# Performance work log

Hardware: AMD Instinct MI355X
Metric: run time of the kernel (lower is better)

The kernel has to match this reference:

```python
import jax, jax.numpy as jnp
import numpy as np

I, H, B, T = 17, 128, 32768, 19

def setup_inputs() -> dict:
    key = jax.random.key(0)
    ks = jax.random.split(key, 7)
    s = 1.0 / np.sqrt(H)  # PyTorch LSTMCell/Linear init scale
    u = lambda k, shape: jax.random.uniform(k, shape, jnp.float32, -s, s)
    return {
        "x": jax.random.normal(ks[0], (B, T, I), jnp.float32),
        "W_ih": u(ks[1], (4 * H, I)),
        "W_hh": u(ks[2], (4 * H, H)),
        "b_ih": u(ks[3], (4 * H,)),
        "b_hh": u(ks[4], (4 * H,)),
        "W_out": u(ks[5], (I, H)),
        "b_out": u(ks[6], (I,)),
    }

def reference(x, W_ih, W_hh, b_ih, b_hh, W_out, b_out):
    B_, T_, _ = x.shape
    Hh = W_hh.shape[1]
    # Precompute input projections for all timesteps in one GEMM: [B,T,4H]
    x_proj = jnp.einsum('bti,gi->btg', x, W_ih) + b_ih + b_hh

    def step(carry, xp_t):
        h, c = carry
        gates = xp_t + h @ W_hh.T            # [B,4H]
        i_g, f_g, g_g, o_g = jnp.split(gates, 4, axis=-1)
        c = jax.nn.sigmoid(f_g) * c + jax.nn.sigmoid(i_g) * jnp.tanh(g_g)
        h = jax.nn.sigmoid(o_g) * jnp.tanh(c)
        y = h @ W_out.T + b_out              # [B,I]
        return (h, c), y

    h0 = jnp.zeros((B_, Hh), x.dtype)
    c0 = jnp.zeros((B_, Hh), x.dtype)
    _, ys = jax.lax.scan(step, (h0, c0), jnp.swapaxes(x_proj, 0, 1))  # ys: [T,B,I]
    return jnp.swapaxes(ys, 0, 1)  # [B,T,I]
```

## Files before the change

### kernel.cpp

```cpp
#include <hip/hip_runtime.h>

#define I_DIM 17
#define H_DIM 128
#define T_DIM 19
#define B_DIM 32768
#define M_ROWS 128
#define NTHR 512
#define GRID (B_DIM / M_ROWS)
#define XI 323
#define NF (M_ROWS * XI)
#define XSLOT 4352

#define GB0 0
#define GB1 16384
#define OFF_X 32768
#define OFF_WO 115456
#define LDS_TOT 123648

typedef __bf16 bf16x8 __attribute__((ext_vector_type(8)));
typedef float f32x4 __attribute__((ext_vector_type(4)));
typedef float f32x4u __attribute__((ext_vector_type(4), aligned(4)));
union FragU { bf16x8 v; unsigned short s[8]; uint4 u; };

#define K1 1.4426950408889634f
#define K2 2.8853900817779268f

__device__ __forceinline__ unsigned short f2bf(float f) {
    union { float f; unsigned u; } x; x.f = f;
    return (unsigned short)((x.u + 0x8000u) >> 16);
}

#define MFMA_Q(QT_, GB_, XB_, XK_, REC_) do {                                     \
    _Pragma("unroll") for (int g = 0; g < 4; ++g)                                 \
        acc[QT_][g] = bias[g];                                                    \
    FragU fx; fx.u = (uint4){0u, 0u, 0u, 0u};                                     \
    if (q < 2)                                                                    \
        fx.v = *(const bf16x8*)(smem + (XB_) + (QT_) * 512);                      \
    else if (q == 2)                                                              \
        fx.s[0] = *(const unsigned short*)(smem + (XK_) + (QT_) * 32);            \
    _Pragma("unroll") for (int g = 0; g < 4; ++g)                                 \
        acc[QT_][g] = __builtin_amdgcn_mfma_f32_16x16x32_bf16(wihr[g], fx.v, acc[QT_][g], 0, 0, 0); \
    if (REC_) {                                                                   \
        _Pragma("unroll") for (int kk = 0; kk < 4; ++kk) {                        \
            bf16x8 a = *(const bf16x8*)(smem + vkk[kk] + ((GB_) + (QT_) * 4096)); \
            _Pragma("unroll") for (int g = 0; g < 4; ++g)                         \
                acc[QT_][g] = __builtin_amdgcn_mfma_f32_16x16x32_bf16(whh[kk][g], a, acc[QT_][g], 0, 0, 0); \
        }                                                                         \
    }                                                                             \
} while (0)

#define ELEM_Q(QT_, GB_, CST_) do {                                               \
    unsigned long long hp = 0ull;                                                 \
    _Pragma("unroll") for (int r = 0; r < 4; ++r) {                               \
        float ui = __builtin_amdgcn_exp2f(acc[QT_][0][r]);                        \
        float uf = __builtin_amdgcn_exp2f(acc[QT_][1][r]);                        \
        float vg = __builtin_amdgcn_exp2f(acc[QT_][2][r]);                        \
        float uo = __builtin_amdgcn_exp2f(acc[QT_][3][r]);                        \
        float A_ = 1.f + ui, F_ = 1.f + uf, G_ = 1.f + vg;                        \
        float AG = A_ * G_;                                                       \
        int ci = (QT_) * 4 + r;                                                   \
        float c = (CST_[ci] * AG + (1.f - vg) * F_) * __builtin_amdgcn_rcpf(F_ * AG); \
        CST_[ci] = c;                                                             \
        float vc = __builtin_amdgcn_exp2f(-K2 * c);                               \
        float h = (1.f - vc) * __builtin_amdgcn_rcpf((1.f + uo) * (1.f + vc));    \
        union { float f; unsigned u; } hu; hu.f = h;                              \
        hp |= (unsigned long long)((hu.u + 0x8000u) >> 16) << (16 * r);           \
    }                                                                             \
    *(unsigned long long*)(smem + vwrT + ((GB_) + (QT_) * 4096)) = hp;            \
} while (0)

#define Y_T(GB_, YP_) do {                                                        \
    f32x4 ya = {0.f, 0.f, 0.f, 0.f};                                              \
    _Pragma("unroll") for (int kk = 0; kk < 4; ++kk) {                            \
        bf16x8 wa = *(const bf16x8*)(smem + vwo + kk * 1024);                     \
        bf16x8 hb = *(const bf16x8*)(smem + vkk[kk] + ((GB_) + 0) + yrt4);        \
        ya = __builtin_amdgcn_mfma_f32_16x16x32_bf16(wa, hb, ya, 0, 0, 0);        \
    }                                                                             \
    if (yct == 0) {                                                               \
        *(f32x4u*)(YP_) = ya + ybo;                                               \
    } else if (q == 0) {                                                          \
        (YP_)[0] = ya[0] + ybo[0];                                                \
    }                                                                             \
} while (0)

__global__ __launch_bounds__(NTHR)
__attribute__((amdgpu_waves_per_eu(2, 2)))
void flowlstm(
    const float* __restrict__ x, const float* __restrict__ W_ih,
    const float* __restrict__ W_hh, const float* __restrict__ b_ih,
    const float* __restrict__ b_hh, const float* __restrict__ W_out,
    const float* __restrict__ b_out, float* __restrict__ out)
{
    __shared__ __align__(16) unsigned char smem[LDS_TOT];
    const int tid = threadIdx.x;
    const int w = tid >> 6, lane = tid & 63, l15 = lane & 15, q = lane >> 4;
    const int cg = w;
    const int b0 = blockIdx.x * M_ROWS;

    {
        const float* xb = x + (size_t)b0 * XI;
        for (int j = 0; j < 81; ++j) {
            int f = tid + j * NTHR;
            if (f < NF) {
                float v = xb[f];
                unsigned uf_ = (unsigned)f;
                unsigned row = (uf_ * 51943u) >> 24;
                unsigned s = uf_ - row * 323u;
                unsigned t = (s * 61681u) >> 20;
                unsigned k = s - t * 17u;
                unsigned a;
                if (k == 16) a = OFF_X + t * XSLOT + 4096 + row * 2;
                else a = OFF_X + t * XSLOT + (row >> 4) * 512 + (k >> 3) * 256
                       + (row & 15) * 16 + (k & 7) * 2;
                *(unsigned short*)(smem + a) = f2bf(v);
            }
        }
    }
    {
        int ln = tid & 63, f = tid >> 6;
        int kk = f & 3, ct = f >> 2;
        int o = ct * 16 + (ln & 15);
        int kb = kk * 32 + (ln >> 4) * 8;
        FragU fu;
        #pragma unroll
        for (int e = 0; e < 8; ++e)
            fu.s[e] = (o < I_DIM) ? f2bf(W_out[o * H_DIM + kb + e]) : (unsigned short)0;
        *(uint4*)(smem + OFF_WO + f * 1024 + ln * 16) = fu.u;
    }
    float gsc[4] = { -K1, -K1, -K2, -K1 };

    bf16x8 whh[4][4];
    #pragma unroll
    for (int kk = 0; kk < 4; ++kk)
        #pragma unroll
        for (int g = 0; g < 4; ++g) {
            int n = g * H_DIM + cg * 16 + l15;
            const float* s = W_hh + n * H_DIM + kk * 32 + q * 8;
            FragU fu;
            #pragma unroll
            for (int e = 0; e < 8; ++e) fu.s[e] = f2bf(s[e] * gsc[g]);
            whh[kk][g] = fu.v;
        }
    bf16x8 wihr[4];
    #pragma unroll
    for (int g = 0; g < 4; ++g) {
        int n = g * H_DIM + cg * 16 + l15;
        FragU fu;
        #pragma unroll
        for (int e = 0; e < 8; ++e) {
            int k = q * 8 + e;
            fu.s[e] = (k < I_DIM) ? f2bf(W_ih[n * I_DIM + k] * gsc[g]) : (unsigned short)0;
        }
        wihr[g] = fu.v;
    }
    f32x4 bias[4];
    #pragma unroll
    for (int g = 0; g < 4; ++g)
        #pragma unroll
        for (int r = 0; r < 4; ++r) {
            int col = g * H_DIM + cg * 16 + 4 * q + r;
            bias[g][r] = (b_ih[col] + b_hh[col]) * gsc[g];
        }
    const unsigned xr7 = (unsigned)((l15 & 7) << 4);
    unsigned vkk[4];
    #pragma unroll
    for (int kk = 0; kk < 4; ++kk)
        vkk[kk] = (unsigned)(l15 * 256 + ((kk * 64 + q * 16) ^ xr7));
    const unsigned vwrT = (unsigned)(l15 * 256 + (((cg * 16 + 4 * q) * 2) ^ xr7));
    const int yct = w & 1;
    const unsigned yrt4 = (unsigned)((w >> 1) * 4096);
    const unsigned vwo = (unsigned)(OFF_WO + yct * 4096 + lane * 16);
    f32x4 ybo;
    #pragma unroll
    for (int r = 0; r < 4; ++r) {
        int col = yct * 16 + 4 * q + r;
        ybo[r] = b_out[col < I_DIM ? col : 16];
    }
    unsigned xyA  = (unsigned)(OFF_X + (q < 2 ? q * 256 : 0) + l15 * 16);
    unsigned xk16 = (unsigned)(OFF_X + 4096 + l15 * 2);
    float* ypG0 = out + (size_t)(b0 + (w >> 1) * 16 + l15) * XI + (yct ? 16 : 4 * q);
    float* ypG1 = ypG0 + (size_t)64 * XI;

    float cstA[16], cstB[16];
    #pragma unroll
    for (int i = 0; i < 16; ++i) { cstA[i] = 0.f; cstB[i] = 0.f; }

    f32x4 acc[4][4];

    __syncthreads();

    MFMA_Q(0, GB0, xyA, xk16, 0);
    MFMA_Q(1, GB0, xyA, xk16, 0);
    MFMA_Q(2, GB0, xyA, xk16, 0);
    MFMA_Q(3, GB0, xyA, xk16, 0);
    __syncthreads();
    ELEM_Q(0, GB0, cstA); MFMA_Q(0, GB1, xyA + 2048, xk16 + 128, 0);
    ELEM_Q(1, GB0, cstA); MFMA_Q(1, GB1, xyA + 2048, xk16 + 128, 0);
    ELEM_Q(2, GB0, cstA); MFMA_Q(2, GB1, xyA + 2048, xk16 + 128, 0);
    ELEM_Q(3, GB0, cstA); MFMA_Q(3, GB1, xyA + 2048, xk16 + 128, 0);
    __syncthreads();
    xyA += XSLOT; xk16 += XSLOT;

    #pragma unroll 1
    for (int k = 1; k < T_DIM; ++k) {
        ELEM_Q(0, GB1, cstB); MFMA_Q(0, GB0, xyA, xk16, 1);
        ELEM_Q(1, GB1, cstB); MFMA_Q(1, GB0, xyA, xk16, 1);
        Y_T(GB0, ypG0);
        ELEM_Q(2, GB1, cstB); MFMA_Q(2, GB0, xyA, xk16, 1);
        ELEM_Q(3, GB1, cstB); MFMA_Q(3, GB0, xyA, xk16, 1);
        __syncthreads();
        ELEM_Q(0, GB0, cstA); MFMA_Q(0, GB1, xyA + 2048, xk16 + 128, 1);
        ELEM_Q(1, GB0, cstA); MFMA_Q(1, GB1, xyA + 2048, xk16 + 128, 1);
        Y_T(GB1, ypG1);
        ELEM_Q(2, GB0, cstA); MFMA_Q(2, GB1, xyA + 2048, xk16 + 128, 1);
        ELEM_Q(3, GB0, cstA); MFMA_Q(3, GB1, xyA + 2048, xk16 + 128, 1);
        __syncthreads();
        xyA += XSLOT; xk16 += XSLOT;
        ypG0 += I_DIM; ypG1 += I_DIM;
    }

    ELEM_Q(0, GB1, cstB);
    ELEM_Q(1, GB1, cstB);
    Y_T(GB0, ypG0);
    ELEM_Q(2, GB1, cstB);
    ELEM_Q(3, GB1, cstB);
    __syncthreads();
    Y_T(GB1, ypG1);
}

extern "C" void kernel_launch(void* const* d_in, const int* in_sizes, int n_in,
                              void* d_out, int out_size, void* d_ws, size_t ws_size,
                              hipStream_t stream) {
    const float* x     = (const float*)d_in[0];
    const float* W_ih  = (const float*)d_in[1];
    const float* W_hh  = (const float*)d_in[2];
    const float* b_ih  = (const float*)d_in[3];
    const float* b_hh  = (const float*)d_in[4];
    const float* W_out = (const float*)d_in[5];
    const float* b_out = (const float*)d_in[6];
    float* out = (float*)d_out;

    dim3 grid(GRID), block(NTHR);
    flowlstm<<<grid, block, 0, stream>>>(x, W_ih, W_hh, b_ih, b_hh, W_out, b_out, out);
}
```

Measured before the change: 151.1 us.

## Halve rows per block, move W_hh into LDS, stream x per timestep

Each block now handles 64 batch rows with 1024 threads instead of 128 rows with 512 threads. W_hh moves from per-wave registers into LDS and is re-read each step. The bias is folded into the W_ih MFMA through a constant-one input column. x is no longer bulk-staged up front; each step prefetches the next timestep into a double-buffered LDS slot. The two interleaved half-batches in flight are replaced by a single step sequence with two barriers per step, aiming for more waves per SIMD and less register pressure, at the cost of extra LDS traffic and more synchronisation.

```diff
diff --git a/kernel.cpp b/kernel.cpp
--- a/kernel.cpp
+++ b/kernel.cpp
@@ -4,18 +4,17 @@
 #define H_DIM 128
 #define T_DIM 19
 #define B_DIM 32768
-#define M_ROWS 128
-#define NTHR 512
+#define M_ROWS 64
+#define NTHR 1024
 #define GRID (B_DIM / M_ROWS)
 #define XI 323
-#define NF (M_ROWS * XI)
-#define XSLOT 4352
-
-#define GB0 0
-#define GB1 16384
-#define OFF_X 32768
-#define OFF_WO 115456
-#define LDS_TOT 123648
+#define XSLOT 2176
+
+#define OFF_WHH 0
+#define OFF_H   131072
+#define OFF_X   147456
+#define OFF_WO  151808
+#define LDS_TOT 160000
 
 typedef __bf16 bf16x8 __attribute__((ext_vector_type(8)));
 typedef float f32x4 __attribute__((ext_vector_type(4)));
@@ -30,61 +29,88 @@
     return (unsigned short)((x.u + 0x8000u) >> 16);
 }
 
-#define MFMA_Q(QT_, GB_, XB_, XK_, REC_) do {                                     \
-    _Pragma("unroll") for (int g = 0; g < 4; ++g)                                 \
-        acc[QT_][g] = bias[g];                                                    \
-    FragU fx; fx.u = (uint4){0u, 0u, 0u, 0u};                                     \
-    if (q < 2)                                                                    \
-        fx.v = *(const bf16x8*)(smem + (XB_) + (QT_) * 512);                      \
-    else if (q == 2)                                                              \
-        fx.s[0] = *(const unsigned short*)(smem + (XK_) + (QT_) * 32);            \
-    _Pragma("unroll") for (int g = 0; g < 4; ++g)                                 \
-        acc[QT_][g] = __builtin_amdgcn_mfma_f32_16x16x32_bf16(wihr[g], fx.v, acc[QT_][g], 0, 0, 0); \
+#define STEP_READ(P_, REC_) do {                                                  \
+    _Pragma("unroll") for (int tile = 0; tile < 2; ++tile) {                      \
+        FragU fx; fx.u = (uint4){0u, 0u, 0u, 0u};                                 \
+        if (q < 2)                                                                \
+            fx.v = *(const bf16x8*)(smem + xyA + ((P_) * XSLOT + tile * 512));    \
+        else if (q == 2) {                                                        \
+            fx.s[0] = *(const unsigned short*)(smem + xk16 + ((P_) * XSLOT + tile * 32)); \
+            fx.s[1] = (unsigned short)0x3F80;                \
+        }                                                                         \
+        _Pragma("unroll") for (int g = 0; g < 4; ++g) {                           \
+            f32x4 z = {0.f, 0.f, 0.f, 0.f};                                       \
+            acc[tile][g] = __builtin_amdgcn_mfma_f32_16x16x32_bf16(wihr[g], fx.v, z, 0, 0, 0); \
+        }                                                                         \
+    }                                                                             \
     if (REC_) {                                                                   \
         _Pragma("unroll") for (int kk = 0; kk < 4; ++kk) {                        \
-            bf16x8 a = *(const bf16x8*)(smem + vkk[kk] + ((GB_) + (QT_) * 4096)); \
+            bf16x8 aw[4];                                                         \
             _Pragma("unroll") for (int g = 0; g < 4; ++g)                         \
-                acc[QT_][g] = __builtin_amdgcn_mfma_f32_16x16x32_bf16(whh[kk][g], a, acc[QT_][g], 0, 0, 0); \
-        }                                                                         \
-    }                                                                             \
-} while (0)
-
-#define ELEM_Q(QT_, GB_, CST_) do {                                               \
+                aw[g] = *(const bf16x8*)(smem + vwhh + (kk * 4096 + g * 1024));   \
+            _Pragma("unroll") for (int tile = 0; tile < 2; ++tile) {              \
+                bf16x8 hb = *(const bf16x8*)(smem + vkk[kk] + tile * 4096);       \
+                _Pragma("unroll") for (int g = 0; g < 4; ++g)                     \
+                    acc[tile][g] = __builtin_amdgcn_mfma_f32_16x16x32_bf16(aw[g], hb, acc[tile][g], 0, 0, 0); \
+            }                                                                     \
+        }                                                                         \
+    }                                                                             \
+} while (0)
+
+#define ELEM_T(TILE_) do {                                                        \
     unsigned long long hp = 0ull;                                                 \
     _Pragma("unroll") for (int r = 0; r < 4; ++r) {                               \
-        float ui = __builtin_amdgcn_exp2f(acc[QT_][0][r]);                        \
-        float uf = __builtin_amdgcn_exp2f(acc[QT_][1][r]);                        \
-        float vg = __builtin_amdgcn_exp2f(acc[QT_][2][r]);                        \
-        float uo = __builtin_amdgcn_exp2f(acc[QT_][3][r]);                        \
+        float ui = __builtin_amdgcn_exp2f(acc[TILE_][0][r]);                      \
+        float uf = __builtin_amdgcn_exp2f(acc[TILE_][1][r]);                      \
+        float vg = __builtin_amdgcn_exp2f(acc[TILE_][2][r]);                      \
+        float uo = __builtin_amdgcn_exp2f(acc[TILE_][3][r]);                      \
         float A_ = 1.f + ui, F_ = 1.f + uf, G_ = 1.f + vg;                        \
         float AG = A_ * G_;                                                       \
-        int ci = (QT_) * 4 + r;                                                   \
-        float c = (CST_[ci] * AG + (1.f - vg) * F_) * __builtin_amdgcn_rcpf(F_ * AG); \
-        CST_[ci] = c;                                                             \
+        int ci = (TILE_) * 4 + r;                                                 \
+        float c = (cst[ci] * AG + (1.f - vg) * F_) * __builtin_amdgcn_rcpf(F_ * AG); \
+        cst[ci] = c;                                                              \
         float vc = __builtin_amdgcn_exp2f(-K2 * c);                               \
         float h = (1.f - vc) * __builtin_amdgcn_rcpf((1.f + uo) * (1.f + vc));    \
         union { float f; unsigned u; } hu; hu.f = h;                              \
         hp |= (unsigned long long)((hu.u + 0x8000u) >> 16) << (16 * r);           \
     }                                                                             \
-    *(unsigned long long*)(smem + vwrT + ((GB_) + (QT_) * 4096)) = hp;            \
-} while (0)
-
-#define Y_T(GB_, YP_) do {                                                        \
-    f32x4 ya = {0.f, 0.f, 0.f, 0.f};                                              \
-    _Pragma("unroll") for (int kk = 0; kk < 4; ++kk) {                            \
-        bf16x8 wa = *(const bf16x8*)(smem + vwo + kk * 1024);                     \
-        bf16x8 hb = *(const bf16x8*)(smem + vkk[kk] + ((GB_) + 0) + yrt4);        \
-        ya = __builtin_amdgcn_mfma_f32_16x16x32_bf16(wa, hb, ya, 0, 0, 0);        \
-    }                                                                             \
-    if (yct == 0) {                                                               \
-        *(f32x4u*)(YP_) = ya + ybo;                                               \
-    } else if (q == 0) {                                                          \
-        (YP_)[0] = ya[0] + ybo[0];                                                \
-    }                                                                             \
+    *(unsigned long long*)(smem + vwrT + (TILE_) * 4096) = hp;                    \
+} while (0)
+
+#define Y_BURST() do {                                                            \
+    if (w < 8) {                                                                  \
+        f32x4 ya = {0.f, 0.f, 0.f, 0.f};                                          \
+        _Pragma("unroll") for (int kk = 0; kk < 4; ++kk) {                        \
+            bf16x8 wa = *(const bf16x8*)(smem + vwo + kk * 1024);                 \
+            bf16x8 hb = *(const bf16x8*)(smem + yv[kk]);                          \
+            ya = __builtin_amdgcn_mfma_f32_16x16x32_bf16(wa, hb, ya, 0, 0, 0);    \
+        }                                                                         \
+        if (yct == 0) {                                                           \
+            *(f32x4u*)ypt = ya + ybo;                                             \
+        } else if (q == 0) {                                                      \
+            ypt[0] = ya[0] + ybo[0];                                              \
+        }                                                                         \
+        ypt += I_DIM;                                                             \
+    }                                                                             \
+} while (0)
+
+#define STEP(T_, P_, REC_) do {                                                   \
+    float xr1 = 0.f, xr2 = 0.f;                                                   \
+    const bool pf = (T_) + 1 < T_DIM;                                             \
+    if (pf) { xr1 = xp1[17]; if (xv2) xr2 = xp2[17]; }                            \
+    xp1 += 17; xp2 += 17;                                                         \
+    STEP_READ(P_, REC_);                                                          \
+    if (REC_) { Y_BURST(); __syncthreads(); }                \
+    ELEM_T(0); ELEM_T(1);                                                         \
+    if (pf) {                                                                     \
+        *(unsigned short*)(smem + xd1 + (1 - (P_)) * XSLOT) = f2bf(xr1);          \
+        if (xv2) *(unsigned short*)(smem + xd2 + (1 - (P_)) * XSLOT) = f2bf(xr2); \
+    }                                                                             \
+    __syncthreads();                                \
 } while (0)
 
 __global__ __launch_bounds__(NTHR)
-__attribute__((amdgpu_waves_per_eu(2, 2)))
+__attribute__((amdgpu_waves_per_eu(4, 4)))
 void flowlstm(
     const float* __restrict__ x, const float* __restrict__ W_ih,
     const float* __restrict__ W_hh, const float* __restrict__ b_ih,
@@ -94,29 +120,23 @@
     __shared__ __align__(16) unsigned char smem[LDS_TOT];
     const int tid = threadIdx.x;
     const int w = tid >> 6, lane = tid & 63, l15 = lane & 15, q = lane >> 4;
-    const int cg = w;
+    const int mh = w >> 3, cg = w & 7;
     const int b0 = blockIdx.x * M_ROWS;
 
-    {
-        const float* xb = x + (size_t)b0 * XI;
-        for (int j = 0; j < 81; ++j) {
-            int f = tid + j * NTHR;
-            if (f < NF) {
-                float v = xb[f];
-                unsigned uf_ = (unsigned)f;
-                unsigned row = (uf_ * 51943u) >> 24;
-                unsigned s = uf_ - row * 323u;
-                unsigned t = (s * 61681u) >> 20;
-                unsigned k = s - t * 17u;
-                unsigned a;
-                if (k == 16) a = OFF_X + t * XSLOT + 4096 + row * 2;
-                else a = OFF_X + t * XSLOT + (row >> 4) * 512 + (k >> 3) * 256
-                       + (row & 15) * 16 + (k & 7) * 2;
-                *(unsigned short*)(smem + a) = f2bf(v);
-            }
-        }
-    }
-    {
+    #pragma unroll
+    for (int i = 0; i < 8; ++i) {
+        int s = tid + i * NTHR;
+        int ln = s & 63, f = s >> 6;
+        int g = f & 3, kk = (f >> 2) & 3, cgs = f >> 4;
+        float sc = (g == 2) ? -K2 : -K1;
+        int n = g * H_DIM + cgs * 16 + (ln & 15);
+        const float* sp = W_hh + n * H_DIM + kk * 32 + (ln >> 4) * 8;
+        FragU fu;
+        #pragma unroll
+        for (int e = 0; e < 8; ++e) fu.s[e] = f2bf(sp[e] * sc);
+        *(uint4*)(smem + OFF_WHH + f * 1024 + ln * 16) = fu.u;
+    }
+    if (tid < 512) {
         int ln = tid & 63, f = tid >> 6;
         int kk = f & 3, ct = f >> 2;
         int o = ct * 16 + (ln & 15);
@@ -127,48 +147,34 @@
             fu.s[e] = (o < I_DIM) ? f2bf(W_out[o * H_DIM + kb + e]) : (unsigned short)0;
         *(uint4*)(smem + OFF_WO + f * 1024 + ln * 16) = fu.u;
     }
-    float gsc[4] = { -K1, -K1, -K2, -K1 };
-
-    bf16x8 whh[4][4];
-    #pragma unroll
-    for (int kk = 0; kk < 4; ++kk)
-        #pragma unroll
-        for (int g = 0; g < 4; ++g) {
-            int n = g * H_DIM + cg * 16 + l15;
-            const float* s = W_hh + n * H_DIM + kk * 32 + q * 8;
-            FragU fu;
-            #pragma unroll
-            for (int e = 0; e < 8; ++e) fu.s[e] = f2bf(s[e] * gsc[g]);
-            whh[kk][g] = fu.v;
-        }
     bf16x8 wihr[4];
     #pragma unroll
     for (int g = 0; g < 4; ++g) {
+        float sc = (g == 2) ? -K2 : -K1;
         int n = g * H_DIM + cg * 16 + l15;
         FragU fu;
         #pragma unroll
         for (int e = 0; e < 8; ++e) {
             int k = q * 8 + e;
-            fu.s[e] = (k < I_DIM) ? f2bf(W_ih[n * I_DIM + k] * gsc[g]) : (unsigned short)0;
+            float v = 0.f;
+            if (k < I_DIM)       v = W_ih[n * I_DIM + k] * sc;
+            else if (k == I_DIM) v = (b_ih[n] + b_hh[n]) * sc;
+            fu.s[e] = f2bf(v);
         }
         wihr[g] = fu.v;
     }
-    f32x4 bias[4];
-    #pragma unroll
-    for (int g = 0; g < 4; ++g)
-        #pragma unroll
-        for (int r = 0; r < 4; ++r) {
-            int col = g * H_DIM + cg * 16 + 4 * q + r;
-            bias[g][r] = (b_ih[col] + b_hh[col]) * gsc[g];
-        }
     const unsigned xr7 = (unsigned)((l15 & 7) << 4);
-    unsigned vkk[4];
+    unsigned vkk[4], yv[4];
     #pragma unroll
     for (int kk = 0; kk < 4; ++kk)
-        vkk[kk] = (unsigned)(l15 * 256 + ((kk * 64 + q * 16) ^ xr7));
-    const unsigned vwrT = (unsigned)(l15 * 256 + (((cg * 16 + 4 * q) * 2) ^ xr7));
+        vkk[kk] = (unsigned)(OFF_H + mh * 8192 + l15 * 256 + ((kk * 64 + q * 16) ^ xr7));
+    const unsigned vwrT = (unsigned)(OFF_H + mh * 8192 + l15 * 256 + (((cg * 16 + 4 * q) * 2) ^ xr7));
+    const unsigned vwhh = (unsigned)(OFF_WHH + cg * 16384 + lane * 16);
     const int yct = w & 1;
-    const unsigned yrt4 = (unsigned)((w >> 1) * 4096);
+    const unsigned ytile = (unsigned)((w >> 1) * 4096);
+    #pragma unroll
+    for (int kk = 0; kk < 4; ++kk)
+        yv[kk] = (unsigned)(OFF_H + ytile + l15 * 256 + ((kk * 64 + q * 16) ^ xr7));
     const unsigned vwo = (unsigned)(OFF_WO + yct * 4096 + lane * 16);
     f32x4 ybo;
     #pragma unroll
@@ -176,56 +182,56 @@
         int col = yct * 16 + 4 * q + r;
         ybo[r] = b_out[col < I_DIM ? col : 16];
     }
-    unsigned xyA  = (unsigned)(OFF_X + (q < 2 ? q * 256 : 0) + l15 * 16);
-    unsigned xk16 = (unsigned)(OFF_X + 4096 + l15 * 2);
-    float* ypG0 = out + (size_t)(b0 + (w >> 1) * 16 + l15) * XI + (yct ? 16 : 4 * q);
-    float* ypG1 = ypG0 + (size_t)64 * XI;
-
-    float cstA[16], cstB[16];
-    #pragma unroll
-    for (int i = 0; i < 16; ++i) { cstA[i] = 0.f; cstB[i] = 0.f; }
-
-    f32x4 acc[4][4];
+    const unsigned xyA  = (unsigned)(OFF_X + mh * 1024 + (q < 2 ? q * 256 : 0) + l15 * 16);
+    const unsigned xk16 = (unsigned)(OFF_X + 2048 + mh * 64 + l15 * 2);
+    float* ypt = out + (size_t)(b0 + (w >> 1) * 16 + l15) * XI + (yct ? 16 : 4 * q);
+
+    const unsigned row1 = ((unsigned)tid * 61681u) >> 20;
+    const unsigned k1 = (unsigned)tid - row1 * 17u;
+    const bool xv2 = tid < (M_ROWS * I_DIM - NTHR);
+    const unsigned f2v = (unsigned)(tid + NTHR);
+    const unsigned row2 = xv2 ? ((f2v * 61681u) >> 20) : 0u;
+    const unsigned k2 = xv2 ? (f2v - row2 * 17u) : 0u;
+    const unsigned xd1 = (k1 == 16) ? (unsigned)(OFF_X + 2048 + row1 * 2)
+        : (unsigned)(OFF_X + (row1 >> 4) * 512 + (k1 >> 3) * 256 + (row1 & 15) * 16 + (k1 & 7) * 2);
+    const unsigned xd2 = (k2 == 16) ? (unsigned)(OFF_X + 2048 + row2 * 2)
+        : (unsigned)(OFF_X + (row2 >> 4) * 512 + (k2 >> 3) * 256 + (row2 & 15) * 16 + (k2 & 7) * 2);
+    const float* xp1 = x + (size_t)(b0 + row1) * XI + k1;
+    const float* xp2 = x + (size_t)(b0 + row2) * XI + k2;
+
+    *(unsigned short*)(smem + xd1) = f2bf(xp1[0]);
+    if (xv2) *(unsigned short*)(smem + xd2) = f2bf(xp2[0]);
+
+    float cst[8];
+    #pragma unroll
+    for (int i = 0; i < 8; ++i) cst[i] = 0.f;
+
+    f32x4 acc[2][4];
 
     __syncthreads();
 
-    MFMA_Q(0, GB0, xyA, xk16, 0);
-    MFMA_Q(1, GB0, xyA, xk16, 0);
-    MFMA_Q(2, GB0, xyA, xk16, 0);
-    MFMA_Q(3, GB0, xyA, xk16, 0);
-    __syncthreads();
-    ELEM_Q(0, GB0, cstA); MFMA_Q(0, GB1, xyA + 2048, xk16 + 128, 0);
-    ELEM_Q(1, GB0, cstA); MFMA_Q(1, GB1, xyA + 2048, xk16 + 128, 0);
-    ELEM_Q(2, GB0, cstA); MFMA_Q(2, GB1, xyA + 2048, xk16 + 128, 0);
-    ELEM_Q(3, GB0, cstA); MFMA_Q(3, GB1, xyA + 2048, xk16 + 128, 0);
-    __syncthreads();
-    xyA += XSLOT; xk16 += XSLOT;
+    STEP(0, 0, 0);
 
     #pragma unroll 1
-    for (int k = 1; k < T_DIM; ++k) {
-        ELEM_Q(0, GB1, cstB); MFMA_Q(0, GB0, xyA, xk16, 1);
-        ELEM_Q(1, GB1, cstB); MFMA_Q(1, GB0, xyA, xk16, 1);
-        Y_T(GB0, ypG0);
-        ELEM_Q(2, GB1, cstB); MFMA_Q(2, GB0, xyA, xk16, 1);
-        ELEM_Q(3, GB1, cstB); MFMA_Q(3, GB0, xyA, xk16, 1);
-        __syncthreads();
-        ELEM_Q(0, GB0, cstA); MFMA_Q(0, GB1, xyA + 2048, xk16 + 128, 1);
-        ELEM_Q(1, GB0, cstA); MFMA_Q(1, GB1, xyA + 2048, xk16 + 128, 1);
-        Y_T(GB1, ypG1);
-        ELEM_Q(2, GB0, cstA); MFMA_Q(2, GB1, xyA + 2048, xk16 + 128, 1);
-        ELEM_Q(3, GB0, cstA); MFMA_Q(3, GB1, xyA + 2048, xk16 + 128, 1);
-        __syncthreads();
-        xyA += XSLOT; xk16 += XSLOT;
-        ypG0 += I_DIM; ypG1 += I_DIM;
-    }
-
-    ELEM_Q(0, GB1, cstB);
-    ELEM_Q(1, GB1, cstB);
-    Y_T(GB0, ypG0);
-    ELEM_Q(2, GB1, cstB);
-    ELEM_Q(3, GB1, cstB);
-    __syncthreads();
-    Y_T(GB1, ypG1);
+    for (int t = 1; t < T_DIM; t += 2) {
+        STEP(t, 1, 1);
+        STEP(t + 1, 0, 1);
+    }
+
+    if (w < 8) {
+        f32x4 ya = {0.f, 0.f, 0.f, 0.f};
+        #pragma unroll
+        for (int kk = 0; kk < 4; ++kk) {
+            bf16x8 wa = *(const bf16x8*)(smem + vwo + kk * 1024);
+            bf16x8 hb = *(const bf16x8*)(smem + yv[kk]);
+            ya = __builtin_amdgcn_mfma_f32_16x16x32_bf16(wa, hb, ya, 0, 0, 0);
+        }
+        if (yct == 0) {
+            *(f32x4u*)ypt = ya + ybo;
+        } else if (q == 0) {
+            ypt[0] = ya[0] + ybo[0];
+        }
+    }
 }
 
 extern "C" void kernel_launch(void* const* d_in, const int* in_sizes, int n_in,
```

Result: slower. 160.5 us (+6.3%).

## Switch LSTM recurrence to 32x32x16 MFMA tiles with single-step h ping-pong

Applied to the files above, without the earlier changes.

Rebuilds the recurrent GEMM around 32x32x16 bf16 MFMA. Each wave owns two 8-column gate slices across all four gates, giving 32-row gate tiles. The bias is folded into the input-projection MFMA through a constant-one K lane. The two interleaved half-batch pipelines are replaced by one full-batch step per barrier, with an h ping-pong buffer. W_out moves from LDS into registers, and the output projection is done once per step over both half-batches. The aim is higher MFMA efficiency and fewer LDS reads and barriers, at the cost of more registers, a larger LDS footprint, and less ILP between the elementwise and MFMA phases.

```diff
diff --git a/kernel.cpp b/kernel.cpp
--- a/kernel.cpp
+++ b/kernel.cpp
@@ -11,14 +11,13 @@
 #define NF (M_ROWS * XI)
 #define XSLOT 4352
 
-#define GB0 0
-#define GB1 16384
-#define OFF_X 32768
-#define OFF_WO 115456
-#define LDS_TOT 123648
+#define OFF_H 0
+#define OFF_X 65536
+#define LDS_TOT 148224
 
 typedef __bf16 bf16x8 __attribute__((ext_vector_type(8)));
 typedef float f32x4 __attribute__((ext_vector_type(4)));
+typedef float f32x16 __attribute__((ext_vector_type(16)));
 typedef float f32x4u __attribute__((ext_vector_type(4), aligned(4)));
 union FragU { bf16x8 v; unsigned short s[8]; uint4 u; };
 
@@ -30,57 +29,94 @@
     return (unsigned short)((x.u + 0x8000u) >> 16);
 }
 
-#define MFMA_Q(QT_, GB_, XB_, XK_, REC_) do {                                     \
-    _Pragma("unroll") for (int g = 0; g < 4; ++g)                                 \
-        acc[QT_][g] = bias[g];                                                    \
-    FragU fx; fx.u = (uint4){0u, 0u, 0u, 0u};                                     \
-    if (q < 2)                                                                    \
-        fx.v = *(const bf16x8*)(smem + (XB_) + (QT_) * 512);                      \
-    else if (q == 2)                                                              \
-        fx.s[0] = *(const unsigned short*)(smem + (XK_) + (QT_) * 32);            \
-    _Pragma("unroll") for (int g = 0; g < 4; ++g)                                 \
-        acc[QT_][g] = __builtin_amdgcn_mfma_f32_16x16x32_bf16(wihr[g], fx.v, acc[QT_][g], 0, 0, 0); \
+#define RB(BT_, P_) do {                                                          \
+    _Pragma("unroll") for (int kk = 0; kk < 8; ++kk)                              \
+        hb[kk] = *(const bf16x8*)(smem + OFF_H + (1 - (P_)) * 32768               \
+                 + ((BT_) * 32 + l31) * 256 + ((kk * 32 + hi * 16) ^ sw15));      \
+} while (0)
+
+#define MQ(BT_, CTI_, ACC_, REC_) do {                                            \
+    FragU f1; f1.v = *(const bf16x8*)(smem + xt + (BT_) * 1024 + lane * 16);      \
+    FragU f2; f2.u = (uint4){0u, 0u, 0u, 0u};                                     \
+    if (hi == 0) {                                                                \
+        f2.s[0] = *(const unsigned short*)(smem + xt + 4096 + ((BT_) * 32 + l31) * 2); \
+        f2.s[1] = (unsigned short)0x3F80;                                         \
+    }                                                                             \
+    f32x16 z = {0.f,0.f,0.f,0.f,0.f,0.f,0.f,0.f,0.f,0.f,0.f,0.f,0.f,0.f,0.f,0.f};\
+    ACC_ = __builtin_amdgcn_mfma_f32_32x32x16_bf16(wihr[CTI_][0], f1.v, z, 0, 0, 0); \
+    ACC_ = __builtin_amdgcn_mfma_f32_32x32x16_bf16(wihr[CTI_][1], f2.v, ACC_, 0, 0, 0); \
     if (REC_) {                                                                   \
-        _Pragma("unroll") for (int kk = 0; kk < 4; ++kk) {                        \
-            bf16x8 a = *(const bf16x8*)(smem + vkk[kk] + ((GB_) + (QT_) * 4096)); \
-            _Pragma("unroll") for (int g = 0; g < 4; ++g)                         \
-                acc[QT_][g] = __builtin_amdgcn_mfma_f32_16x16x32_bf16(whh[kk][g], a, acc[QT_][g], 0, 0, 0); \
-        }                                                                         \
-    }                                                                             \
-} while (0)
-
-#define ELEM_Q(QT_, GB_, CST_) do {                                               \
+        _Pragma("unroll") for (int kk = 0; kk < 8; ++kk)                          \
+            ACC_ = __builtin_amdgcn_mfma_f32_32x32x16_bf16(whh[CTI_][kk], hb[kk], ACC_, 0, 0, 0); \
+    }                                                                             \
+} while (0)
+
+#define EQ(ACC_, TI_, CTI_, BT_, P_) do {                                         \
     unsigned long long hp = 0ull;                                                 \
-    _Pragma("unroll") for (int r = 0; r < 4; ++r) {                               \
-        float ui = __builtin_amdgcn_exp2f(acc[QT_][0][r]);                        \
-        float uf = __builtin_amdgcn_exp2f(acc[QT_][1][r]);                        \
-        float vg = __builtin_amdgcn_exp2f(acc[QT_][2][r]);                        \
-        float uo = __builtin_amdgcn_exp2f(acc[QT_][3][r]);                        \
+    _Pragma("unroll") for (int jj = 0; jj < 4; ++jj) {                            \
+        float ui = __builtin_amdgcn_exp2f(ACC_[jj]);                              \
+        float uf = __builtin_amdgcn_exp2f(ACC_[4 + jj]);                          \
+        float vg = __builtin_amdgcn_exp2f(ACC_[8 + jj]);                          \
+        float uo = __builtin_amdgcn_exp2f(ACC_[12 + jj]);                         \
         float A_ = 1.f + ui, F_ = 1.f + uf, G_ = 1.f + vg;                        \
         float AG = A_ * G_;                                                       \
-        int ci = (QT_) * 4 + r;                                                   \
-        float c = (CST_[ci] * AG + (1.f - vg) * F_) * __builtin_amdgcn_rcpf(F_ * AG); \
-        CST_[ci] = c;                                                             \
+        int ci = (TI_) * 4 + jj;                                                  \
+        float c = (cst[ci] * AG + (1.f - vg) * F_) * __builtin_amdgcn_rcpf(F_ * AG); \
+        cst[ci] = c;                                                              \
         float vc = __builtin_amdgcn_exp2f(-K2 * c);                               \
         float h = (1.f - vc) * __builtin_amdgcn_rcpf((1.f + uo) * (1.f + vc));    \
         union { float f; unsigned u; } hu; hu.f = h;                              \
-        hp |= (unsigned long long)((hu.u + 0x8000u) >> 16) << (16 * r);           \
-    }                                                                             \
-    *(unsigned long long*)(smem + vwrT + ((GB_) + (QT_) * 4096)) = hp;            \
-} while (0)
-
-#define Y_T(GB_, YP_) do {                                                        \
-    f32x4 ya = {0.f, 0.f, 0.f, 0.f};                                              \
+        hp |= (unsigned long long)((hu.u + 0x8000u) >> 16) << (16 * jj);          \
+    }                                                                             \
+    *(unsigned long long*)(smem + OFF_H + (P_) * 32768 + ((BT_) * 32 + l31) * 256 \
+        + (((2 * w + (CTI_)) * 16 + hi * 8) ^ sw15)) = hp;                        \
+} while (0)
+
+#define YB(P_) do {                                                               \
+    f32x4 ya0 = {0.f,0.f,0.f,0.f}, ya1 = {0.f,0.f,0.f,0.f};                       \
     _Pragma("unroll") for (int kk = 0; kk < 4; ++kk) {                            \
-        bf16x8 wa = *(const bf16x8*)(smem + vwo + kk * 1024);                     \
-        bf16x8 hb = *(const bf16x8*)(smem + vkk[kk] + ((GB_) + 0) + yrt4);        \
-        ya = __builtin_amdgcn_mfma_f32_16x16x32_bf16(wa, hb, ya, 0, 0, 0);        \
+        bf16x8 h0 = *(const bf16x8*)(smem + OFF_H + (1 - (P_)) * 32768            \
+                   + (ybt * 16 + l15) * 256 + ((kk * 64 + q * 16) ^ (l15 << 4))); \
+        bf16x8 h1 = *(const bf16x8*)(smem + OFF_H + (1 - (P_)) * 32768            \
+                   + ((ybt + 4) * 16 + l15) * 256 + ((kk * 64 + q * 16) ^ (l15 << 4))); \
+        ya0 = __builtin_amdgcn_mfma_f32_16x16x32_bf16(wor[kk], h0, ya0, 0, 0, 0); \
+        ya1 = __builtin_amdgcn_mfma_f32_16x16x32_bf16(wor[kk], h1, ya1, 0, 0, 0); \
     }                                                                             \
     if (yct == 0) {                                                               \
-        *(f32x4u*)(YP_) = ya + ybo;                                               \
+        *(f32x4u*)ypt0 = ya0 + ybo;                                               \
+        *(f32x4u*)ypt1 = ya1 + ybo;                                               \
     } else if (q == 0) {                                                          \
-        (YP_)[0] = ya[0] + ybo[0];                                                \
-    }                                                                             \
+        ypt0[0] = ya0[0] + ybo[0];                                                \
+        ypt1[0] = ya1[0] + ybo[0];                                                \
+    }                                                                             \
+    ypt0 += I_DIM; ypt1 += I_DIM;                                                 \
+} while (0)
+
+#define STEP(P_, REC_) do {                                                       \
+    bf16x8 hb[8];                                                                 \
+    if (REC_) RB(0, P_);                                                          \
+    MQ(0, 0, accA, REC_);                                                         \
+    MQ(0, 1, accB, REC_);                                                         \
+    if (REC_) RB(1, P_);                                                          \
+    EQ(accA, 0, 0, 0, P_);                                                        \
+    MQ(1, 0, accA, REC_);                                                         \
+    EQ(accB, 1, 1, 0, P_);                                                        \
+    MQ(1, 1, accB, REC_);                                                         \
+    if (REC_) RB(2, P_);                                                          \
+    EQ(accA, 2, 0, 1, P_);                                                        \
+    MQ(2, 0, accA, REC_);                                                         \
+    EQ(accB, 3, 1, 1, P_);                                                        \
+    MQ(2, 1, accB, REC_);                                                         \
+    if (REC_) YB(P_);                                                             \
+    if (REC_) RB(3, P_);                                                          \
+    EQ(accA, 4, 0, 2, P_);                                                        \
+    MQ(3, 0, accA, REC_);                                                         \
+    EQ(accB, 5, 1, 2, P_);                                                        \
+    MQ(3, 1, accB, REC_);                                                         \
+    EQ(accA, 6, 0, 3, P_);                                                        \
+    EQ(accB, 7, 1, 3, P_);                                                        \
+    xt += XSLOT;                                                                  \
+    __syncthreads();                                                              \
 } while (0)
 
 __global__ __launch_bounds__(NTHR)
@@ -93,8 +129,9 @@
 {
     __shared__ __align__(16) unsigned char smem[LDS_TOT];
     const int tid = threadIdx.x;
-    const int w = tid >> 6, lane = tid & 63, l15 = lane & 15, q = lane >> 4;
-    const int cg = w;
+    const int w = tid >> 6, lane = tid & 63;
+    const int l31 = lane & 31, hi = lane >> 5, l15 = lane & 15, q = lane >> 4;
+    const unsigned sw15 = (unsigned)((l31 & 15) << 4);
     const int b0 = blockIdx.x * M_ROWS;
 
     {
@@ -109,123 +146,84 @@
                 unsigned t = (s * 61681u) >> 20;
                 unsigned k = s - t * 17u;
                 unsigned a;
-                if (k == 16) a = OFF_X + t * XSLOT + 4096 + row * 2;
-                else a = OFF_X + t * XSLOT + (row >> 4) * 512 + (k >> 3) * 256
-                       + (row & 15) * 16 + (k & 7) * 2;
+                if (k == 16u)
+                    a = OFF_X + t * XSLOT + 4096 + row * 2;
+                else
+                    a = OFF_X + t * XSLOT + (row >> 5) * 1024
+                      + (((k >> 3) * 32 + (row & 31)) * 16) + (k & 7) * 2;
                 *(unsigned short*)(smem + a) = f2bf(v);
             }
         }
     }
-    {
-        int ln = tid & 63, f = tid >> 6;
-        int kk = f & 3, ct = f >> 2;
-        int o = ct * 16 + (ln & 15);
-        int kb = kk * 32 + (ln >> 4) * 8;
+    bf16x8 whh[2][8];
+    const int jrow = l31 & 7, grow = l31 >> 3;
+    const float scl = (grow == 2) ? -K2 : -K1;
+    #pragma unroll
+    for (int cti = 0; cti < 2; ++cti) {
+        int n = grow * H_DIM + (2 * w + cti) * 8 + jrow;
+        #pragma unroll
+        for (int kk = 0; kk < 8; ++kk) {
+            const float* sp = W_hh + n * H_DIM + kk * 16 + hi * 8;
+            FragU fu;
+            #pragma unroll
+            for (int e = 0; e < 8; ++e) fu.s[e] = f2bf(sp[e] * scl);
+            whh[cti][kk] = fu.v;
+        }
+    }
+    bf16x8 wihr[2][2];
+    #pragma unroll
+    for (int cti = 0; cti < 2; ++cti) {
+        int n = grow * H_DIM + (2 * w + cti) * 8 + jrow;
+        FragU fa, fb;
+        #pragma unroll
+        for (int e = 0; e < 8; ++e) {
+            int k0 = hi * 8 + e;
+            fa.s[e] = f2bf(W_ih[n * I_DIM + k0] * scl);
+            int k1 = 16 + hi * 8 + e;
+            float v = 0.f;
+            if (k1 == 16)      v = W_ih[n * I_DIM + 16] * scl;
+            else if (k1 == 17) v = (b_ih[n] + b_hh[n]) * scl;
+            fb.s[e] = f2bf(v);
+        }
+        wihr[cti][0] = fa.v;
+        wihr[cti][1] = fb.v;
+    }
+    const int ybt = w >> 1, yct = w & 1;
+    const int ycol = yct * 16 + l15;
+    bf16x8 wor[4];
+    #pragma unroll
+    for (int kk = 0; kk < 4; ++kk) {
         FragU fu;
         #pragma unroll
         for (int e = 0; e < 8; ++e)
-            fu.s[e] = (o < I_DIM) ? f2bf(W_out[o * H_DIM + kb + e]) : (unsigned short)0;
-        *(uint4*)(smem + OFF_WO + f * 1024 + ln * 16) = fu.u;
-    }
-    float gsc[4] = { -K1, -K1, -K2, -K1 };
-
-    bf16x8 whh[4][4];
-    #pragma unroll
-    for (int kk = 0; kk < 4; ++kk)
-        #pragma unroll
-        for (int g = 0; g < 4; ++g) {
-            int n = g * H_DIM + cg * 16 + l15;
-            const float* s = W_hh + n * H_DIM + kk * 32 + q * 8;
-            FragU fu;
-            #pragma unroll
-            for (int e = 0; e < 8; ++e) fu.s[e] = f2bf(s[e] * gsc[g]);
-            whh[kk][g] = fu.v;
-        }
-    bf16x8 wihr[4];
-    #pragma unroll
-    for (int g = 0; g < 4; ++g) {
-        int n = g * H_DIM + cg * 16 + l15;
-        FragU fu;
-        #pragma unroll
-        for (int e = 0; e < 8; ++e) {
-            int k = q * 8 + e;
-            fu.s[e] = (k < I_DIM) ? f2bf(W_ih[n * I_DIM + k] * gsc[g]) : (unsigned short)0;
-        }
-        wihr[g] = fu.v;
-    }
-    f32x4 bias[4];
-    #pragma unroll
-    for (int g = 0; g < 4; ++g)
-        #pragma unroll
-        for (int r = 0; r < 4; ++r) {
-            int col = g * H_DIM + cg * 16 + 4 * q + r;
-            bias[g][r] = (b_ih[col] + b_hh[col]) * gsc[g];
-        }
-    const unsigned xr7 = (unsigned)((l15 & 7) << 4);
-    unsigned vkk[4];
-    #pragma unroll
-    for (int kk = 0; kk < 4; ++kk)
-        vkk[kk] = (unsigned)(l15 * 256 + ((kk * 64 + q * 16) ^ xr7));
-    const unsigned vwrT = (unsigned)(l15 * 256 + (((cg * 16 + 4 * q) * 2) ^ xr7));
-    const int yct = w & 1;
-    const unsigned yrt4 = (unsigned)((w >> 1) * 4096);
-    const unsigned vwo = (unsigned)(OFF_WO + yct * 4096 + lane * 16);
+            fu.s[e] = (ycol < I_DIM) ? f2bf(W_out[ycol * H_DIM + kk * 32 + q * 8 + e])
+                                     : (unsigned short)0;
+        wor[kk] = fu.v;
+    }
     f32x4 ybo;
     #pragma unroll
     for (int r = 0; r < 4; ++r) {
         int col = yct * 16 + 4 * q + r;
         ybo[r] = b_out[col < I_DIM ? col : 16];
     }
-    unsigned xyA  = (unsigned)(OFF_X + (q < 2 ? q * 256 : 0) + l15 * 16);
-    unsigned xk16 = (unsigned)(OFF_X + 4096 + l15 * 2);
-    float* ypG0 = out + (size_t)(b0 + (w >> 1) * 16 + l15) * XI + (yct ? 16 : 4 * q);
-    float* ypG1 = ypG0 + (size_t)64 * XI;
-
-    float cstA[16], cstB[16];
-    #pragma unroll
-    for (int i = 0; i < 16; ++i) { cstA[i] = 0.f; cstB[i] = 0.f; }
-
-    f32x4 acc[4][4];
+    float* ypt0 = out + (size_t)(b0 + ybt * 16 + l15) * XI + (yct ? 16 : 4 * q);
+    float* ypt1 = ypt0 + (size_t)64 * XI;
+
+    float cst[32];
+    #pragma unroll
+    for (int i = 0; i < 32; ++i) cst[i] = 0.f;
+    f32x16 accA, accB;
+    unsigned xt = OFF_X;
 
     __syncthreads();
 
-    MFMA_Q(0, GB0, xyA, xk16, 0);
-    MFMA_Q(1, GB0, xyA, xk16, 0);
-    MFMA_Q(2, GB0, xyA, xk16, 0);
-    MFMA_Q(3, GB0, xyA, xk16, 0);
-    __syncthreads();
-    ELEM_Q(0, GB0, cstA); MFMA_Q(0, GB1, xyA + 2048, xk16 + 128, 0);
-    ELEM_Q(1, GB0, cstA); MFMA_Q(1, GB1, xyA + 2048, xk16 + 128, 0);
-    ELEM_Q(2, GB0, cstA); MFMA_Q(2, GB1, xyA + 2048, xk16 + 128, 0);
-    ELEM_Q(3, GB0, cstA); MFMA_Q(3, GB1, xyA + 2048, xk16 + 128, 0);
-    __syncthreads();
-    xyA += XSLOT; xk16 += XSLOT;
-
+    STEP(0, 0);
     #pragma unroll 1
-    for (int k = 1; k < T_DIM; ++k) {
-        ELEM_Q(0, GB1, cstB); MFMA_Q(0, GB0, xyA, xk16, 1);
-        ELEM_Q(1, GB1, cstB); MFMA_Q(1, GB0, xyA, xk16, 1);
-        Y_T(GB0, ypG0);
-        ELEM_Q(2, GB1, cstB); MFMA_Q(2, GB0, xyA, xk16, 1);
-        ELEM_Q(3, GB1, cstB); MFMA_Q(3, GB0, xyA, xk16, 1);
-        __syncthreads();
-        ELEM_Q(0, GB0, cstA); MFMA_Q(0, GB1, xyA + 2048, xk16 + 128, 1);
-        ELEM_Q(1, GB0, cstA); MFMA_Q(1, GB1, xyA + 2048, xk16 + 128, 1);
-        Y_T(GB1, ypG1);
-        ELEM_Q(2, GB0, cstA); MFMA_Q(2, GB1, xyA + 2048, xk16 + 128, 1);
-        ELEM_Q(3, GB0, cstA); MFMA_Q(3, GB1, xyA + 2048, xk16 + 128, 1);
-        __syncthreads();
-        xyA += XSLOT; xk16 += XSLOT;
-        ypG0 += I_DIM; ypG1 += I_DIM;
-    }
-
-    ELEM_Q(0, GB1, cstB);
-    ELEM_Q(1, GB1, cstB);
-    Y_T(GB0, ypG0);
-    ELEM_Q(2, GB1, cstB);
-    ELEM_Q(3, GB1, cstB);
-    __syncthreads();
-    Y_T(GB1, ypG1);
+    for (int t = 1; t < T_DIM; t += 2) {
+        STEP(1, 1);
+        STEP(0, 1);
+    }
+    YB(1);
 }
 
 extern "C" void kernel_launch(void* const* d_in, const int* in_sizes, int n_in,
```

Measured after the change: 153.8 us. Within noise of the previous version (+1.8%).
